# Performance work log

Hardware: AMD Instinct MI355X
Metric: run time of the kernel (lower is better)

## Reference

```python
import jax, jax.numpy as jnp
import numpy as np

SCENE_SHAPE = (128, 128, 8)
C, HEADS, LEVELS, POINTS = 128, 8, 3, 4
HEAD_DIM = C // HEADS
FEAT_SHAPES = ((47, 153), (24, 77), (12, 39))
B = 2


def setup_inputs():
    key = jax.random.key(0)
    ks = jax.random.split(key, 16)
    N = SCENE_SHAPE[0] * SCENE_SHAPE[1] * SCENE_SHAPE[2]
    s = 1.0 / np.sqrt(C)
    inp = {
        "scene_embed": jax.random.normal(ks[0], (B, N, C), jnp.float32),
        "scene_pos": jax.random.normal(ks[1], (B, N, C), jnp.float32) * 0.02,
        "vol_pts": jax.random.randint(ks[2], (B, N, 3), 0, 140),
        "ref_pix": jax.random.uniform(ks[3], (B, N, 2), jnp.float32),
        "Wv": jax.random.normal(ks[7], (C, C), jnp.float32) * s,
        "bv": jnp.zeros((C,), jnp.float32),
        "Woff": jax.random.normal(ks[8], (C, HEADS * LEVELS * POINTS * 2), jnp.float32) * 0.01,
        "boff": jax.random.normal(ks[9], (HEADS * LEVELS * POINTS * 2,), jnp.float32) * 0.5,
        "Ww": jax.random.normal(ks[10], (C, HEADS * LEVELS * POINTS), jnp.float32) * s,
        "bw": jnp.zeros((HEADS * LEVELS * POINTS,), jnp.float32),
        "Wo": jax.random.normal(ks[11], (C, C), jnp.float32) * s,
        "bo": jnp.zeros((C,), jnp.float32),
        "ln_g": jnp.ones((C,), jnp.float32),
        "ln_b": jnp.zeros((C,), jnp.float32),
    }
    for l, (h, w) in enumerate(FEAT_SHAPES):
        inp[f"feat{l}"] = jax.random.normal(ks[4 + l], (B, C, h, w), jnp.float32)
    return inp


def _deform_attn_layer(query, query_pos, feats, ref_pix, Wv, bv, Woff, boff, Ww, bw, Wo, bo, ln_g, ln_b):
    # mmcv MultiScaleDeformableAttention (+ residual) followed by LayerNorm
    Bq, Nq, _ = query.shape
    identity = query
    q = query + query_pos
    # flatten multi-scale feats -> [B, sum(HW), C], then value projection
    value = jnp.concatenate([f.reshape(Bq, C, -1).transpose(0, 2, 1) for f in feats], axis=1) @ Wv + bv
    offsets = (q @ Woff + boff).reshape(Bq, Nq, HEADS, LEVELS, POINTS, 2)
    attw = jax.nn.softmax((q @ Ww + bw).reshape(Bq, Nq, HEADS, LEVELS * POINTS), axis=-1)
    attw = attw.reshape(Bq, Nq, HEADS, LEVELS, POINTS)
    acc = jnp.zeros((Bq, HEADS, Nq, HEAD_DIM), query.dtype)
    start = 0
    for l, (h, w) in enumerate(FEAT_SHAPES):
        # per-level value: [B, heads, H*W, head_dim]
        v_l = value[:, start:start + h * w].reshape(Bq, h * w, HEADS, HEAD_DIM).transpose(0, 2, 1, 3)
        start += h * w
        norm = jnp.array([w, h], query.dtype)  # offset normalizer order (W, H)
        for p in range(POINTS):
            loc = ref_pix[:, :, None, :] + offsets[:, :, :, l, p, :] / norm  # [B,Nq,heads,2] in [0,1] (x,y)
            x = loc[..., 0] * w - 0.5  # grid_sample align_corners=False
            y = loc[..., 1] * h - 0.5
            x0 = jnp.floor(x)
            y0 = jnp.floor(y)
            fx = x - x0
            fy = y - y0
            x0i = x0.astype(jnp.int32)
            y0i = y0.astype(jnp.int32)
            samp = jnp.zeros((Bq, HEADS, Nq, HEAD_DIM), query.dtype)
            for dy, dx, cw in ((0, 0, (1 - fx) * (1 - fy)), (0, 1, fx * (1 - fy)),
                               (1, 0, (1 - fx) * fy), (1, 1, fx * fy)):
                xi = x0i + dx
                yi = y0i + dy
                valid = (xi >= 0) & (xi < w) & (yi >= 0) & (yi < h)  # zero padding outside
                idx = jnp.clip(yi, 0, h - 1) * w + jnp.clip(xi, 0, w - 1)
                g = jnp.take_along_axis(v_l, idx.transpose(0, 2, 1)[..., None], axis=2)  # [B,heads,Nq,D]
                samp = samp + g * (cw * valid).transpose(0, 2, 1)[..., None]
            acc = acc + samp * attw[:, :, :, l, p].transpose(0, 2, 1)[..., None]
    out = acc.transpose(0, 2, 1, 3).reshape(Bq, Nq, C) @ Wo + bo + identity
    mu = out.mean(-1, keepdims=True)
    var = ((out - mu) ** 2).mean(-1, keepdims=True)
    return (out - mu) / jnp.sqrt(var + 1e-5) * ln_g + ln_b


def reference(scene_embed, scene_pos, vol_pts, ref_pix, feat0, feat1, feat2,
              Wv, bv, Woff, boff, Ww, bw, Wo, bo, ln_g, ln_b):
    X, Y, Z = SCENE_SHAPE
    N = X * Y * Z
    Bq = scene_embed.shape[0]
    keep = ((vol_pts[..., 0] >= 0) & (vol_pts[..., 0] < X)
            & (vol_pts[..., 1] >= 0) & (vol_pts[..., 1] < Y)
            & (vol_pts[..., 2] >= 0) & (vol_pts[..., 2] < Z))
    flat = jnp.where(keep, vol_pts[..., 0] * (Y * Z) + vol_pts[..., 1] * Z + vol_pts[..., 2], 0)
    # pts_mask[b, v] = True iff some in-bounds vol_pt of sample b hits voxel v
    pts_mask = jnp.zeros((Bq, N), bool).at[jnp.arange(Bq)[:, None], flat].max(keep)
    # deformable attn is per-query independent (and LayerNorm is per-token), so computing it on
    # all N queries then selecting with the mask is mathematically identical to the torch
    # gather -> attend -> scatter-back, without dynamic shapes.
    pts_embed = _deform_attn_layer(scene_embed, scene_pos, (feat0, feat1, feat2), ref_pix,
                                   Wv, bv, Woff, boff, Ww, bw, Wo, bo, ln_g, ln_b)
    out = jnp.where(pts_mask[..., None], pts_embed, scene_embed)  # index_fov_back_to_voxels
    return out.transpose(0, 2, 1).reshape(Bq, C, X, Y, Z)
```

## Files before the change

### kernel.cpp

```cpp
#include <hip/hip_runtime.h>
#include <hip/hip_bf16.h>
#include <stdint.h>

#define B_Q     2
#define N_TOK   131072
#define S_VAL   9507
#define PROW    292
#define TROW    36

typedef __attribute__((ext_vector_type(8))) short short8;
typedef __attribute__((ext_vector_type(4))) short short4v;
typedef __attribute__((ext_vector_type(4))) float f32x4;

__device__ __forceinline__ unsigned short f32_bf16(float f) {
    unsigned u = __float_as_uint(f);
    u += 0x7FFFu + ((u >> 16) & 1u);
    return (unsigned short)(u >> 16);
}
__device__ __forceinline__ float bf16_f32(unsigned short h) {
    return __uint_as_float((unsigned)h << 16);
}

__global__ __launch_bounds__(256) void mask_scatter_kernel(
    const int* __restrict__ vol, int* __restrict__ mask)
{
    int i = blockIdx.x * 256 + threadIdx.x;
    if (i >= B_Q * N_TOK) return;
    int b = i / N_TOK;
    const int* p = vol + (size_t)i * 3;
    int x = p[0], y = p[1], z = p[2];
    if (x >= 0 && x < 128 && y >= 0 && y < 128 && z >= 0 && z < 8)
        mask[b * N_TOK + x * 1024 + y * 8 + z] = 1;
}

__global__ __launch_bounds__(256) void pack_weights_kernel(
    const float* __restrict__ Woff, const float* __restrict__ boff,
    const float* __restrict__ Ww,   const float* __restrict__ bw,
    const float* __restrict__ Wo,
    unsigned short* __restrict__ wcatp, unsigned short* __restrict__ wop,
    float* __restrict__ bias288)
{
    int idx = blockIdx.x * 256 + threadIdx.x;
    if (idx < 36864) {
        int j = idx & 7, l = (idx >> 3) & 63, ks = (idx >> 9) & 3, nt = idx >> 11;
        int n = nt * 16 + (l & 15);
        int k = ks * 32 + (l >> 4) * 8 + j;
        float v = (n < 192) ? Woff[k * 192 + n] : Ww[k * 96 + (n - 192)];
        wcatp[idx] = f32_bf16(v);
    } else if (idx < 53248) {
        int i2 = idx - 36864;
        int j = i2 & 7, l = (i2 >> 3) & 63, ks = (i2 >> 9) & 3, nt = i2 >> 11;
        int n = nt * 16 + (l & 15);
        int k = ks * 32 + (l >> 4) * 8 + j;
        wop[i2] = f32_bf16(Wo[k * 128 + n]);
    } else if (idx < 53536) {
        int i2 = idx - 53248;
        bias288[i2] = (i2 < 192) ? boff[i2] : bw[i2 - 192];
    }
}

__global__ __launch_bounds__(256) void value_proj_kernel(
    const float* __restrict__ f0, const float* __restrict__ f1,
    const float* __restrict__ f2,
    const float* __restrict__ Wv, const float* __restrict__ bv,
    __hip_bfloat16* __restrict__ value)
{
    __shared__ float Ast[128 * 68];

    int blk = blockIdx.x;
    int b   = blk / 149;
    int s0  = (blk % 149) * 64;
    int t   = threadIdx.x;

    int j = t & 63;
    int a = t >> 6;
    int s = s0 + j;
    #pragma unroll
    for (int i = 0; i < 32; ++i) {
        int k = a + 4 * i;
        float v = 0.f;
        if (s < S_VAL) {
            if (s < 7191)      v = f0[((size_t)b * 128 + k) * 7191 + s];
            else if (s < 9039) v = f1[((size_t)b * 128 + k) * 1848 + (s - 7191)];
            else               v = f2[((size_t)b * 128 + k) * 468  + (s - 9039)];
        }
        Ast[k * 68 + j] = v;
    }
    __syncthreads();

    int c  = t & 127;
    int rg = t >> 7;
    float acc[32];
    #pragma unroll
    for (int i = 0; i < 32; ++i) acc[i] = 0.f;

    for (int k = 0; k < 128; ++k) {
        float wv = Wv[k * 128 + c];
        const float4* arow = (const float4*)&Ast[k * 68 + rg * 32];
        #pragma unroll
        for (int ii = 0; ii < 8; ++ii) {
            float4 av = arow[ii];
            acc[4 * ii + 0] += av.x * wv;
            acc[4 * ii + 1] += av.y * wv;
            acc[4 * ii + 2] += av.z * wv;
            acc[4 * ii + 3] += av.w * wv;
        }
    }
    float bvc = bv[c];
    #pragma unroll
    for (int i = 0; i < 32; ++i) {
        int s2 = s0 + rg * 32 + i;
        if (s2 < S_VAL)
            value[((size_t)b * S_VAL + s2) * 128 + c] = __float2bfloat16(acc[i] + bvc);
    }
}

__global__ __launch_bounds__(256, 5) void fused_kernel(
    const float* __restrict__ embed, const float* __restrict__ pos,
    const float* __restrict__ refpix,
    const unsigned short* __restrict__ wcatp,
    const unsigned short* __restrict__ wop,
    const float* __restrict__ bias288,
    const float* __restrict__ bo,
    const float* __restrict__ ln_g, const float* __restrict__ ln_b,
    const __hip_bfloat16* __restrict__ value,
    const int* __restrict__ mask,
    float* __restrict__ out)
{
    __shared__ short qA[4096];
    __shared__ __align__(16) char r2[32 * PROW * 2];

    unsigned short* Pb  = (unsigned short*)r2;
    float*          u2t = (float*)r2;
    short8*         qA8 = (short8*)qA;

    int t     = threadIdx.x;
    int bb    = blockIdx.x;
    int b     = bb >> 12;
    int tbase = (bb & 4095) * 32;
    int lane  = t & 63;
    int wvid  = t >> 6;

    {
        const float4* e4 = (const float4*)(embed + ((size_t)b * N_TOK + tbase) * 128);
        const float4* p4 = (const float4*)(pos   + ((size_t)b * N_TOK + tbase) * 128);
        #pragma unroll
        for (int i = 0; i < 4; ++i) {
            int idx = t + 256 * i;
            int r = idx >> 5, k4 = idx & 31;
            float4 e = e4[idx];
            float4 p = p4[idx];
            short4v q;
            q.x = (short)f32_bf16(e.x + p.x);
            q.y = (short)f32_bf16(e.y + p.y);
            q.z = (short)f32_bf16(e.z + p.z);
            q.w = (short)f32_bf16(e.w + p.w);
            int kg = k4 >> 1;
            int mt = r >> 4, ks = kg >> 2;
            int lpos = (r & 15) + ((kg & 3) << 4);
            short4v* dst = (short4v*)((char*)qA +
                (((size_t)(mt * 4 + ks) * 64 + lpos) * 16 + (k4 & 1) * 8));
            *dst = q;
        }
    }
    __syncthreads();

    {
        int mt = wvid & 1;
        int n0 = (wvid >> 1) * 9;
        f32x4 acc[9];
        #pragma unroll
        for (int i = 0; i < 9; ++i) acc[i] = (f32x4)(0.f);
        const short8* bp = (const short8*)wcatp;
        #pragma unroll
        for (int ks = 0; ks < 4; ++ks) {
            short8 af = qA8[(mt * 4 + ks) * 64 + lane];
            #pragma unroll
            for (int i = 0; i < 9; ++i) {
                short8 bf = bp[((n0 + i) * 4 + ks) * 64 + lane];
                acc[i] = __builtin_amdgcn_mfma_f32_16x16x32_bf16(af, bf, acc[i], 0, 0, 0);
            }
        }
        int col = lane & 15, quad = lane >> 4;
        #pragma unroll
        for (int i = 0; i < 9; ++i) {
            int n = (n0 + i) * 16 + col;
            float bsv = bias288[n];
            #pragma unroll
            for (int reg = 0; reg < 4; ++reg) {
                int row = mt * 16 + quad * 4 + reg;
                Pb[row * PROW + n] = f32_bf16(acc[i][reg] + bsv);
            }
        }
    }
    __syncthreads();

    {
        int r = t >> 3, h = t & 7;
        unsigned short* pw = &Pb[r * PROW + 192 + h * 12];
        float e[12];
        #pragma unroll
        for (int i = 0; i < 12; ++i) e[i] = bf16_f32(pw[i]);
        float mx = e[0];
        #pragma unroll
        for (int i = 1; i < 12; ++i) mx = fmaxf(mx, e[i]);
        float ssum = 0.f;
        #pragma unroll
        for (int i = 0; i < 12; ++i) { e[i] = __expf(e[i] - mx); ssum += e[i]; }
        float inv = 1.f / ssum;
        #pragma unroll
        for (int i = 0; i < 12; ++i) pw[i] = f32_bf16(e[i] * inv);
    }

    {
        int r = t >> 3, h = t & 7;
        int n = tbase + r;
        float2 rp = ((const float2*)refpix)[(size_t)b * N_TOK + n];
        float acc16[16];
        #pragma unroll
        for (int i = 0; i < 16; ++i) acc16[i] = 0.f;

        const unsigned short* pr = &Pb[r * PROW];
        const int LH[3] = {47, 24, 12};
        const int LW[3] = {153, 77, 39};
        const int LS[3] = {0, 7191, 9039};

        #pragma unroll
        for (int l = 0; l < 3; ++l) {
            const int w  = LW[l];
            const int hh = LH[l];
            float bx = rp.x * (float)w  - 0.5f;
            float by = rp.y * (float)hh - 0.5f;
            const __hip_bfloat16* vbase =
                value + ((size_t)b * S_VAL + LS[l]) * 128 + h * 16;
            #pragma unroll
            for (int p = 0; p < 4; ++p) {
                float ox = bf16_f32(pr[((h * 3 + l) * 4 + p) * 2 + 0]);
                float oy = bf16_f32(pr[((h * 3 + l) * 4 + p) * 2 + 1]);
                float aw = bf16_f32(pr[192 + h * 12 + l * 4 + p]);
                float x = bx + ox;
                float y = by + oy;
                float x0f = floorf(x), y0f = floorf(y);
                float fx = x - x0f, fy = y - y0f;
                int x0 = (int)x0f, y0 = (int)y0f;
                #pragma unroll
                for (int tap = 0; tap < 4; ++tap) {
                    int dx = tap & 1, dy = tap >> 1;
                    int xi = x0 + dx, yi = y0 + dy;
                    if (xi >= 0 && xi < w && yi >= 0 && yi < hh) {
                        float cw = (dx ? fx : 1.f - fx) * (dy ? fy : 1.f - fy) * aw;
                        const uint4* vp = (const uint4*)(vbase + (size_t)(yi * w + xi) * 128);
                        uint4 qa = vp[0];
                        uint4 qb = vp[1];
#define ACC2(u, i0) do { \
    acc16[i0]     = fmaf(__uint_as_float((u) << 16),         cw, acc16[i0]); \
    acc16[i0 + 1] = fmaf(__uint_as_float((u) & 0xffff0000u), cw, acc16[i0 + 1]); } while (0)
                        ACC2(qa.x, 0);  ACC2(qa.y, 2);  ACC2(qa.z, 4);  ACC2(qa.w, 6);
                        ACC2(qb.x, 8);  ACC2(qb.y, 10); ACC2(qb.z, 12); ACC2(qb.w, 14);
#undef ACC2
                    }
                }
            }
        }
        short8 v0, v1;
        #pragma unroll
        for (int j2 = 0; j2 < 8; ++j2) {
            v0[j2] = (short)f32_bf16(acc16[j2]);
            v1[j2] = (short)f32_bf16(acc16[8 + j2]);
        }
        int mt = r >> 4, rl = r & 15;
        int kg0 = 2 * h, kg1 = 2 * h + 1;
        qA8[(mt * 4 + (kg0 >> 2)) * 64 + rl + ((kg0 & 3) << 4)] = v0;
        qA8[(mt * 4 + (kg1 >> 2)) * 64 + rl + ((kg1 & 3) << 4)] = v1;
    }
    __syncthreads();

    {
        int mt  = wvid & 1;
        int nt0 = (wvid >> 1) * 4;
        f32x4 acc[4];
        #pragma unroll
        for (int i = 0; i < 4; ++i) acc[i] = (f32x4)(0.f);
        const short8* bp = (const short8*)wop;
        #pragma unroll
        for (int ks = 0; ks < 4; ++ks) {
            short8 af = qA8[(mt * 4 + ks) * 64 + lane];
            #pragma unroll
            for (int i = 0; i < 4; ++i) {
                short8 bf = bp[((nt0 + i) * 4 + ks) * 64 + lane];
                acc[i] = __builtin_amdgcn_mfma_f32_16x16x32_bf16(af, bf, acc[i], 0, 0, 0);
            }
        }
        int col = lane & 15, quad = lane >> 4;
        #pragma unroll
        for (int i = 0; i < 4; ++i) {
            int c = (nt0 + i) * 16 + col;
            float bc = bo[c];
            #pragma unroll
            for (int reg = 0; reg < 4; ++reg) {
                int row = mt * 16 + quad * 4 + reg;
                u2t[c * TROW + row] = acc[i][reg] + bc;
            }
        }
    }
    __syncthreads();

    {
        int r = t >> 3, j = t & 7;
        int n = tbase + r;
        const float* eb = embed + ((size_t)b * N_TOK + n) * 128;
        float v[16], ev[16];
        float s1 = 0.f, s2 = 0.f;
        #pragma unroll
        for (int i = 0; i < 16; ++i) {
            int c = j + 8 * i;
            float e = eb[c];
            float x = u2t[c * TROW + r] + e;
            ev[i] = e; v[i] = x;
            s1 += x; s2 += x * x;
        }
        #pragma unroll
        for (int m = 1; m < 8; m <<= 1) {
            s1 += __shfl_xor(s1, m, 64);
            s2 += __shfl_xor(s2, m, 64);
        }
        float mu   = s1 * (1.f / 128.f);
        float var  = s2 * (1.f / 128.f) - mu * mu;
        float rstd = rsqrtf(var + 1e-5f);
        int   msk  = mask[(size_t)b * N_TOK + n];
        #pragma unroll
        for (int i = 0; i < 16; ++i) {
            int c = j + 8 * i;
            float yv = (v[i] - mu) * rstd * ln_g[c] + ln_b[c];
            u2t[c * TROW + r] = msk ? yv : ev[i];
        }
    }
    __syncthreads();

    {
        #pragma unroll
        for (int i = 0; i < 4; ++i) {
            int idx = t + 256 * i;
            int c = idx >> 3, r4 = idx & 7;
            float4 vv = *(const float4*)&u2t[c * TROW + r4 * 4];
            *(float4*)&out[((size_t)(b * 128 + c)) * N_TOK + tbase + r4 * 4] = vv;
        }
    }
}

extern "C" void kernel_launch(void* const* d_in, const int* in_sizes, int n_in,
                              void* d_out, int out_size, void* d_ws, size_t ws_size,
                              hipStream_t stream)
{
    (void)n_in; (void)out_size; (void)ws_size;

    const float* embed = (const float*)d_in[0];
    const float* posp  = (const float*)d_in[1];
    const int*   vol   = (const int*)  d_in[2];
    const float* refp  = (const float*)d_in[3];

    int iW, iF;
    if (in_sizes[4] == 128 * 128) { iW = 4; iF = 14; }
    else                          { iF = 4; iW = 7;  }

    const float* Wv   = (const float*)d_in[iW + 0];
    const float* bv   = (const float*)d_in[iW + 1];
    const float* Woff = (const float*)d_in[iW + 2];
    const float* boff = (const float*)d_in[iW + 3];
    const float* Ww   = (const float*)d_in[iW + 4];
    const float* bw   = (const float*)d_in[iW + 5];
    const float* Wo   = (const float*)d_in[iW + 6];
    const float* bo   = (const float*)d_in[iW + 7];
    const float* lng  = (const float*)d_in[iW + 8];
    const float* lnb  = (const float*)d_in[iW + 9];
    const float* f0   = (const float*)d_in[iF + 0];
    const float* f1   = (const float*)d_in[iF + 1];
    const float* f2   = (const float*)d_in[iF + 2];

    char* ws = (char*)d_ws;
    int*            maskbuf = (int*)ws;
    __hip_bfloat16* value   = (__hip_bfloat16*)(ws + 1048576);
    unsigned short* wcatp   = (unsigned short*)(ws + 1048576 + 4867584);
    unsigned short* wop     = (unsigned short*)(ws + 1048576 + 4867584 + 73728);
    float*          bias288 = (float*)(ws + 1048576 + 4867584 + 73728 + 32768);

    hipMemsetAsync(maskbuf, 0, (size_t)B_Q * N_TOK * sizeof(int), stream);
    mask_scatter_kernel<<<(B_Q * N_TOK + 255) / 256, 256, 0, stream>>>(vol, maskbuf);
    pack_weights_kernel<<<(53536 + 255) / 256, 256, 0, stream>>>(
        Woff, boff, Ww, bw, Wo, wcatp, wop, bias288);
    value_proj_kernel<<<B_Q * 149, 256, 0, stream>>>(f0, f1, f2, Wv, bv, value);
    fused_kernel<<<B_Q * 4096, 256, 0, stream>>>(
        embed, posp, refp, wcatp, wop, bias288, bo, lng, lnb,
        value, maskbuf, (float*)d_out);
}
```

Measured before the change: 731.5 us.

## Use head-major value layout, branchless bilinear gather, fused softmax, merged aux kernels

Stores projected values in a head-major [B, head, S, 16] bf16 layout, so each head's 16-channel gather touches a contiguous 32-byte row. The bilinear sampling now clamps coordinates and zeroes the weights of out-of-bounds taps, issuing all four tap loads unconditionally instead of branching per tap. Softmax moves into registers inside the sampling phase, which removes a shared-memory write-back pass. The mask scatter and weight-packing kernels merge into one launch, and the value projection uses smaller 32-row tiles to launch more blocks. In exchange, edge taps now issue redundant clamped loads.

```diff
diff --git a/kernel.cpp b/kernel.cpp
--- a/kernel.cpp
+++ b/kernel.cpp
@@ -21,26 +21,26 @@
     return __uint_as_float((unsigned)h << 16);
 }
 
-__global__ __launch_bounds__(256) void mask_scatter_kernel(
-    const int* __restrict__ vol, int* __restrict__ mask)
-{
-    int i = blockIdx.x * 256 + threadIdx.x;
-    if (i >= B_Q * N_TOK) return;
-    int b = i / N_TOK;
-    const int* p = vol + (size_t)i * 3;
-    int x = p[0], y = p[1], z = p[2];
-    if (x >= 0 && x < 128 && y >= 0 && y < 128 && z >= 0 && z < 8)
-        mask[b * N_TOK + x * 1024 + y * 8 + z] = 1;
-}
-
-__global__ __launch_bounds__(256) void pack_weights_kernel(
+__global__ __launch_bounds__(256) void aux_kernel(
+    const int* __restrict__ vol, int* __restrict__ mask,
     const float* __restrict__ Woff, const float* __restrict__ boff,
     const float* __restrict__ Ww,   const float* __restrict__ bw,
     const float* __restrict__ Wo,
     unsigned short* __restrict__ wcatp, unsigned short* __restrict__ wop,
     float* __restrict__ bias288)
 {
-    int idx = blockIdx.x * 256 + threadIdx.x;
+    int blk = blockIdx.x;
+    int t   = threadIdx.x;
+    if (blk < 1024) {
+        int i = blk * 256 + t;
+        int b = i >> 17;
+        const int* p = vol + (size_t)i * 3;
+        int x = p[0], y = p[1], z = p[2];
+        if (x >= 0 && x < 128 && y >= 0 && y < 128 && z >= 0 && z < 8)
+            mask[b * N_TOK + x * 1024 + y * 8 + z] = 1;
+        return;
+    }
+    int idx = (blk - 1024) * 256 + t;
     if (idx < 36864) {
         int j = idx & 7, l = (idx >> 3) & 63, ks = (idx >> 9) & 3, nt = idx >> 11;
         int n = nt * 16 + (l & 15);
@@ -63,42 +63,42 @@
     const float* __restrict__ f0, const float* __restrict__ f1,
     const float* __restrict__ f2,
     const float* __restrict__ Wv, const float* __restrict__ bv,
-    __hip_bfloat16* __restrict__ value)
+    unsigned short* __restrict__ value)
 {
-    __shared__ float Ast[128 * 68];
+    __shared__ float Ast[128 * 36];
 
     int blk = blockIdx.x;
-    int b   = blk / 149;
-    int s0  = (blk % 149) * 64;
+    int b   = blk / 298;
+    int s0  = (blk % 298) * 32;
     int t   = threadIdx.x;
 
-    int j = t & 63;
-    int a = t >> 6;
+    int j = t & 31;
+    int a = t >> 5;
     int s = s0 + j;
     #pragma unroll
-    for (int i = 0; i < 32; ++i) {
-        int k = a + 4 * i;
+    for (int i = 0; i < 16; ++i) {
+        int k = a + 8 * i;
         float v = 0.f;
         if (s < S_VAL) {
             if (s < 7191)      v = f0[((size_t)b * 128 + k) * 7191 + s];
             else if (s < 9039) v = f1[((size_t)b * 128 + k) * 1848 + (s - 7191)];
             else               v = f2[((size_t)b * 128 + k) * 468  + (s - 9039)];
         }
-        Ast[k * 68 + j] = v;
+        Ast[k * 36 + j] = v;
     }
     __syncthreads();
 
     int c  = t & 127;
     int rg = t >> 7;
-    float acc[32];
+    float acc[16];
     #pragma unroll
-    for (int i = 0; i < 32; ++i) acc[i] = 0.f;
+    for (int i = 0; i < 16; ++i) acc[i] = 0.f;
 
     for (int k = 0; k < 128; ++k) {
         float wv = Wv[k * 128 + c];
-        const float4* arow = (const float4*)&Ast[k * 68 + rg * 32];
-        #pragma unroll
-        for (int ii = 0; ii < 8; ++ii) {
+        const float4* arow = (const float4*)&Ast[k * 36 + rg * 16];
+        #pragma unroll
+        for (int ii = 0; ii < 4; ++ii) {
             float4 av = arow[ii];
             acc[4 * ii + 0] += av.x * wv;
             acc[4 * ii + 1] += av.y * wv;
@@ -107,11 +107,12 @@
         }
     }
     float bvc = bv[c];
+    int h = c >> 4, ch = c & 15;
     #pragma unroll
-    for (int i = 0; i < 32; ++i) {
-        int s2 = s0 + rg * 32 + i;
+    for (int i = 0; i < 16; ++i) {
+        int s2 = s0 + rg * 16 + i;
         if (s2 < S_VAL)
-            value[((size_t)b * S_VAL + s2) * 128 + c] = __float2bfloat16(acc[i] + bvc);
+            value[((size_t)(b * 8 + h) * S_VAL + s2) * 16 + ch] = f32_bf16(acc[i] + bvc);
     }
 }
 
@@ -123,7 +124,7 @@
     const float* __restrict__ bias288,
     const float* __restrict__ bo,
     const float* __restrict__ ln_g, const float* __restrict__ ln_b,
-    const __hip_bfloat16* __restrict__ value,
+    const unsigned short* __restrict__ value,
     const int* __restrict__ mask,
     float* __restrict__ out)
 {
@@ -197,30 +198,33 @@
 
     {
         int r = t >> 3, h = t & 7;
-        unsigned short* pw = &Pb[r * PROW + 192 + h * 12];
-        float e[12];
-        #pragma unroll
-        for (int i = 0; i < 12; ++i) e[i] = bf16_f32(pw[i]);
-        float mx = e[0];
-        #pragma unroll
-        for (int i = 1; i < 12; ++i) mx = fmaxf(mx, e[i]);
-        float ssum = 0.f;
-        #pragma unroll
-        for (int i = 0; i < 12; ++i) { e[i] = __expf(e[i] - mx); ssum += e[i]; }
-        float inv = 1.f / ssum;
-        #pragma unroll
-        for (int i = 0; i < 12; ++i) pw[i] = f32_bf16(e[i] * inv);
-    }
-
-    {
-        int r = t >> 3, h = t & 7;
         int n = tbase + r;
         float2 rp = ((const float2*)refpix)[(size_t)b * N_TOK + n];
+        const unsigned short* pr = &Pb[r * PROW];
+
+        uint2 ofs2[6], lg2[3];
+        #pragma unroll
+        for (int i = 0; i < 6; ++i)
+            ofs2[i] = *(const uint2*)(pr + h * 24 + i * 4);
+        #pragma unroll
+        for (int i = 0; i < 3; ++i)
+            lg2[i] = *(const uint2*)(pr + 192 + h * 12 + i * 4);
+        const unsigned short* ofs = (const unsigned short*)ofs2;
+        const unsigned short* lg  = (const unsigned short*)lg2;
+
+        float wgt[12];
+        float mx = -1e30f;
+        #pragma unroll
+        for (int i = 0; i < 12; ++i) { wgt[i] = bf16_f32(lg[i]); mx = fmaxf(mx, wgt[i]); }
+        float ssum = 0.f;
+        #pragma unroll
+        for (int i = 0; i < 12; ++i) { wgt[i] = __expf(wgt[i] - mx); ssum += wgt[i]; }
+        float sinv = 1.f / ssum;
+
         float acc16[16];
         #pragma unroll
         for (int i = 0; i < 16; ++i) acc16[i] = 0.f;
 
-        const unsigned short* pr = &Pb[r * PROW];
         const int LH[3] = {47, 24, 12};
         const int LW[3] = {153, 77, 39};
         const int LS[3] = {0, 7191, 9039};
@@ -231,35 +235,46 @@
             const int hh = LH[l];
             float bx = rp.x * (float)w  - 0.5f;
             float by = rp.y * (float)hh - 0.5f;
-            const __hip_bfloat16* vbase =
-                value + ((size_t)b * S_VAL + LS[l]) * 128 + h * 16;
+            const unsigned short* vb = value + ((size_t)(b * 8 + h) * S_VAL + LS[l]) * 16;
             #pragma unroll
             for (int p = 0; p < 4; ++p) {
-                float ox = bf16_f32(pr[((h * 3 + l) * 4 + p) * 2 + 0]);
-                float oy = bf16_f32(pr[((h * 3 + l) * 4 + p) * 2 + 1]);
-                float aw = bf16_f32(pr[192 + h * 12 + l * 4 + p]);
+                float ox = bf16_f32(ofs[(l * 4 + p) * 2 + 0]);
+                float oy = bf16_f32(ofs[(l * 4 + p) * 2 + 1]);
+                float aw = wgt[l * 4 + p] * sinv;
                 float x = bx + ox;
                 float y = by + oy;
                 float x0f = floorf(x), y0f = floorf(y);
                 float fx = x - x0f, fy = y - y0f;
                 int x0 = (int)x0f, y0 = (int)y0f;
-                #pragma unroll
-                for (int tap = 0; tap < 4; ++tap) {
-                    int dx = tap & 1, dy = tap >> 1;
-                    int xi = x0 + dx, yi = y0 + dy;
-                    if (xi >= 0 && xi < w && yi >= 0 && yi < hh) {
-                        float cw = (dx ? fx : 1.f - fx) * (dy ? fy : 1.f - fy) * aw;
-                        const uint4* vp = (const uint4*)(vbase + (size_t)(yi * w + xi) * 128);
-                        uint4 qa = vp[0];
-                        uint4 qb = vp[1];
-#define ACC2(u, i0) do { \
+                int x1 = x0 + 1,   y1 = y0 + 1;
+                int xc0 = min(max(x0, 0), w - 1),  xc1 = min(max(x1, 0), w - 1);
+                int yc0 = min(max(y0, 0), hh - 1), yc1 = min(max(y1, 0), hh - 1);
+                float wx0 = (x0 < 0 || x0 >= w)  ? 0.f : (1.f - fx);
+                float wx1 = (x1 < 0 || x1 >= w)  ? 0.f : fx;
+                float wy0 = (y0 < 0 || y0 >= hh) ? 0.f : (1.f - fy);
+                float wy1 = (y1 < 0 || y1 >= hh) ? 0.f : fy;
+                float w00 = wx0 * wy0 * aw, w01 = wx1 * wy0 * aw;
+                float w10 = wx0 * wy1 * aw, w11 = wx1 * wy1 * aw;
+                const uint4* t00 = (const uint4*)(vb + (size_t)(yc0 * w + xc0) * 16);
+                const uint4* t01 = (const uint4*)(vb + (size_t)(yc0 * w + xc1) * 16);
+                const uint4* t10 = (const uint4*)(vb + (size_t)(yc1 * w + xc0) * 16);
+                const uint4* t11 = (const uint4*)(vb + (size_t)(yc1 * w + xc1) * 16);
+                uint4 a0 = t00[0], a1 = t00[1];
+                uint4 b0 = t01[0], b1 = t01[1];
+                uint4 c0 = t10[0], c1 = t10[1];
+                uint4 d0 = t11[0], d1 = t11[1];
+#define ACC2(u, cw, i0) do { \
     acc16[i0]     = fmaf(__uint_as_float((u) << 16),         cw, acc16[i0]); \
     acc16[i0 + 1] = fmaf(__uint_as_float((u) & 0xffff0000u), cw, acc16[i0 + 1]); } while (0)
-                        ACC2(qa.x, 0);  ACC2(qa.y, 2);  ACC2(qa.z, 4);  ACC2(qa.w, 6);
-                        ACC2(qb.x, 8);  ACC2(qb.y, 10); ACC2(qb.z, 12); ACC2(qb.w, 14);
+                ACC2(a0.x, w00, 0); ACC2(a0.y, w00, 2); ACC2(a0.z, w00, 4); ACC2(a0.w, w00, 6);
+                ACC2(a1.x, w00, 8); ACC2(a1.y, w00,10); ACC2(a1.z, w00,12); ACC2(a1.w, w00,14);
+                ACC2(b0.x, w01, 0); ACC2(b0.y, w01, 2); ACC2(b0.z, w01, 4); ACC2(b0.w, w01, 6);
+                ACC2(b1.x, w01, 8); ACC2(b1.y, w01,10); ACC2(b1.z, w01,12); ACC2(b1.w, w01,14);
+                ACC2(c0.x, w10, 0); ACC2(c0.y, w10, 2); ACC2(c0.z, w10, 4); ACC2(c0.w, w10, 6);
+                ACC2(c1.x, w10, 8); ACC2(c1.y, w10,10); ACC2(c1.z, w10,12); ACC2(c1.w, w10,14);
+                ACC2(d0.x, w11, 0); ACC2(d0.y, w11, 2); ACC2(d0.z, w11, 4); ACC2(d0.w, w11, 6);
+                ACC2(d1.x, w11, 8); ACC2(d1.y, w11,10); ACC2(d1.z, w11,12); ACC2(d1.w, w11,14);
 #undef ACC2
-                    }
-                }
             }
         }
         short8 v0, v1;
@@ -379,16 +394,15 @@
 
     char* ws = (char*)d_ws;
     int*            maskbuf = (int*)ws;
-    __hip_bfloat16* value   = (__hip_bfloat16*)(ws + 1048576);
+    unsigned short* value   = (unsigned short*)(ws + 1048576);
     unsigned short* wcatp   = (unsigned short*)(ws + 1048576 + 4867584);
     unsigned short* wop     = (unsigned short*)(ws + 1048576 + 4867584 + 73728);
     float*          bias288 = (float*)(ws + 1048576 + 4867584 + 73728 + 32768);
 
     hipMemsetAsync(maskbuf, 0, (size_t)B_Q * N_TOK * sizeof(int), stream);
-    mask_scatter_kernel<<<(B_Q * N_TOK + 255) / 256, 256, 0, stream>>>(vol, maskbuf);
-    pack_weights_kernel<<<(53536 + 255) / 256, 256, 0, stream>>>(
-        Woff, boff, Ww, bw, Wo, wcatp, wop, bias288);
-    value_proj_kernel<<<B_Q * 149, 256, 0, stream>>>(f0, f1, f2, Wv, bv, value);
+    aux_kernel<<<1234, 256, 0, stream>>>(vol, maskbuf, Woff, boff, Ww, bw, Wo,
+                                         wcatp, wop, bias288);
+    value_proj_kernel<<<B_Q * 298, 256, 0, stream>>>(f0, f1, f2, Wv, bv, value);
     fused_kernel<<<B_Q * 4096, 256, 0, stream>>>(
         embed, posp, refp, wcatp, wop, bias288, bo, lng, lnb,
         value, maskbuf, (float*)d_out);
```

Measured after the change: 2.164 ms. +195.9%, slower.
